# Kernel optimization log

Hardware: AMD Instinct MI355X
Metric: run time of the kernel (lower is better)

## Reference

```python
import jax, jax.numpy as jnp
import numpy as np

HEADS = 8
BLOCK = 32

def setup_inputs() -> dict:
    key = jax.random.key(0)
    ks = jax.random.split(key, 4)
    b, n, d, f = 4, 4096, 1024, 128
    x = jax.random.normal(ks[0], (b, n, d), dtype=jnp.float32)
    w_qkv = jax.random.normal(ks[1], (3 * d, d), dtype=jnp.float32) * (d ** -0.5)
    w_out = jax.random.normal(ks[2], (d, d), dtype=jnp.float32) * (d ** -0.5)
    b_out = jnp.zeros((d,), dtype=jnp.float32)
    proj = jax.random.normal(ks[3], (HEADS, d // HEADS, f), dtype=jnp.float32) * ((d // HEADS) ** -0.5)
    return {"x": x, "w_qkv": w_qkv, "w_out": w_out, "b_out": b_out, "proj": proj}

def reference(x, w_qkv, w_out, b_out, proj):
    b, n, d = x.shape
    h = HEADS
    hd = d // h
    nb = n // BLOCK
    # QKV projection (torch Linear: x @ W.T)
    qkv = x @ w_qkv.T  # (b, n, 3d)
    q, k, v = jnp.split(qkv, 3, axis=-1)
    def to_blocks(t):
        # (b, n, d) -> (b, h, nb, BLOCK, hd)
        return t.reshape(b, n, h, hd).transpose(0, 2, 1, 3).reshape(b, h, nb, BLOCK, hd)
    q, k, v = to_blocks(q), to_blocks(k), to_blocks(v)
    # per-head feature map: elu(x @ proj) + 1
    qp = jax.nn.elu(jnp.einsum('bhcsd,hdf->bhcsf', q, proj)) + 1.0
    kp = jax.nn.elu(jnp.einsum('bhcsd,hdf->bhcsf', k, proj)) + 1.0
    # per-block kv state and normalizer
    kv = jnp.einsum('bhcsf,bhcsd->bhcfd', kp, v)          # (b,h,nb,f,hd)
    num = jnp.einsum('bhcsf,bhcfd->bhcsd', qp, kv)        # (b,h,nb,BLOCK,hd)
    ksum = kp.sum(axis=3)                                 # (b,h,nb,f)
    z = 1.0 / (jnp.einsum('bhcsf,bhcf->bhcs', qp, ksum) + 1e-8)
    out = num * z[..., None]
    # merge blocks and heads: (b,h,nb,BLOCK,hd) -> (b,n,d)
    out = out.reshape(b, h, n, hd).transpose(0, 2, 1, 3).reshape(b, n, d)
    # output projection (dropout inert in eval)
    return out @ w_out.T + b_out
```

## Files before the change

kernel.cpp:

```cpp
#include <hip/hip_runtime.h>
#include <hip/hip_bf16.h>
#include <stdint.h>
#include <stddef.h>

typedef __bf16 bf16_t;
typedef __bf16 bf16x8 __attribute__((ext_vector_type(8)));
typedef __bf16 bf16x4 __attribute__((ext_vector_type(4)));
typedef float  f32x4  __attribute__((ext_vector_type(4)));

static __device__ __forceinline__ f32x4 mfma16x16x32(bf16x8 a, bf16x8 b, f32x4 c) {
  return __builtin_amdgcn_mfma_f32_16x16x32_bf16(a, b, c, 0, 0, 0);
}

static __device__ __forceinline__ void gld_lds16(const void* g, void* l) {
  __builtin_amdgcn_global_load_lds(
      (const __attribute__((address_space(1))) unsigned int*)g,
      (__attribute__((address_space(3))) unsigned int*)l, 16, 0, 0);
}

#define BARW()   __builtin_amdgcn_s_barrier()
#define SCHED0() __builtin_amdgcn_sched_barrier(0)
#define LGKM0()  asm volatile("s_waitcnt lgkmcnt(0)" ::: "memory")
#define LGKMN(n) asm volatile("s_waitcnt lgkmcnt(" #n ")" ::: "memory")
#define VMCNT(n) asm volatile("s_waitcnt vmcnt(" #n ")" ::: "memory")
#define PRIO(p)  __builtin_amdgcn_s_setprio(p)

__global__ __launch_bounds__(256) void cvt_bf16(const float* __restrict__ in,
                                                bf16_t* __restrict__ out, int n) {
  int stride = gridDim.x * blockDim.x;
  for (int i = blockIdx.x * blockDim.x + threadIdx.x; i * 4 < n; i += stride) {
    float4 v = *(const float4*)(in + (size_t)i * 4);
    bf16x4 o;
    o[0] = (bf16_t)v.x; o[1] = (bf16_t)v.y; o[2] = (bf16_t)v.z; o[3] = (bf16_t)v.w;
    *(bf16x4*)(out + (size_t)i * 4) = o;
  }
}

__global__ __launch_bounds__(256) void prep(const float* __restrict__ wqkv,
                                            const float* __restrict__ proj,
                                            const float* __restrict__ wout,
                                            bf16_t* __restrict__ B1t2,
                                            bf16_t* __restrict__ Wv,
                                            bf16_t* __restrict__ W3t) {
  const int b = blockIdx.x;
  const int tid = threadIdx.x;
  if (b >= 256) {
    const float* src = (b < 512) ? wout : (wqkv + (size_t)2048 * 1024);
    bf16_t* dst = (b < 512) ? W3t : Wv;
    size_t off = ((size_t)((b & 255)) * 4096) + tid * 16;
#pragma unroll
    for (int it = 0; it < 4; ++it) {
      float4 v = *(const float4*)(src + off + it * 4);
      bf16x4 o;
      o[0] = (bf16_t)v.x; o[1] = (bf16_t)v.y; o[2] = (bf16_t)v.z; o[3] = (bf16_t)v.w;
      *(bf16x4*)(dst + off + it * 4) = o;
    }
    return;
  }
  const int combo  = b >> 4;
  const int kt     = b & 15;
  const int qk     = combo >> 3;
  const int h      = combo & 7;
  const int klocal = tid & 63;
  const int fg     = tid >> 6;
  const int k      = kt * 64 + klocal;

  const float* wbase = wqkv + ((size_t)(qk * 1024 + h * 128)) * 1024 + k;
  const float* pbase = proj + (size_t)h * 16384 + fg * 32;

  float acc[32];
#pragma unroll
  for (int i = 0; i < 32; ++i) acc[i] = 0.f;

  for (int c = 0; c < 128; ++c) {
    float a = wbase[(size_t)c * 1024];
    const float4* p = (const float4*)(pbase + (size_t)c * 128);
#pragma unroll
    for (int i = 0; i < 8; ++i) {
      float4 pv = p[i];
      acc[i * 4 + 0] += a * pv.x;
      acc[i * 4 + 1] += a * pv.y;
      acc[i * 4 + 2] += a * pv.z;
      acc[i * 4 + 3] += a * pv.w;
    }
  }
  bf16_t* obase = B1t2 + ((size_t)(h * 256 + qk * 128 + fg * 32)) * 1024 + k;
#pragma unroll
  for (int i = 0; i < 32; ++i) obase[(size_t)i * 1024] = (bf16_t)acc[i];
}

#define GEMM_MAINLOOP_DECLS()                                                  \
  const int tid  = threadIdx.x;                                                \
  const int lane = tid & 63;                                                   \
  const int wid  = tid >> 6;                                                   \
  const int wm   = wid >> 2;                                                   \
  const int wn   = wid & 3;                                                    \
  const int lr   = lane & 15;                                                  \
  const int g0   = lane >> 4;                                                  \
  int srow[2], sgl[2];                                                         \
  _Pragma("unroll")                                                            \
  for (int l = 0; l < 2; ++l) {                                                \
    int idx = l * 512 + tid;                                                   \
    srow[l] = idx >> 3;                                                        \
    sgl[l]  = (idx & 7) ^ (srow[l] & 7);                                       \
  }

#define STAGE_T(arr, base, half, kt, K_)                                       \
  {                                                                            \
    const bf16_t* s_ = (base) + (size_t)((half) * 128) * (K_) + (kt) * 64;     \
    bf16_t* d_ = &(arr)[half][0];                                              \
    _Pragma("unroll")                                                          \
    for (int l_ = 0; l_ < 2; ++l_)                                             \
      gld_lds16(s_ + (size_t)srow[l_] * (K_) + sgl[l_] * 8,                    \
                d_ + (l_ * 512 + tid) * 8);                                    \
  }

#define RD_A(buf, qm)                                                          \
  _Pragma("unroll")                                                            \
  for (int t_ = 0; t_ < 4; ++t_) {                                             \
    int r_ = (qm) * 64 + t_ * 16 + lr;                                         \
    _Pragma("unroll")                                                          \
    for (int kh_ = 0; kh_ < 2; ++kh_) {                                        \
      int gl_ = (g0 + kh_ * 4) ^ (r_ & 7);                                     \
      a[t_][kh_] = *(const bf16x8*)(&sA[buf][wm][r_ * 64 + gl_ * 8]);          \
    }                                                                          \
  }
#define RD_B(buf, qn, breg)                                                    \
  _Pragma("unroll")                                                            \
  for (int u_ = 0; u_ < 2; ++u_) {                                             \
    int r_ = (wn & 1) * 64 + (qn) * 32 + u_ * 16 + lr;                         \
    _Pragma("unroll")                                                          \
    for (int kh_ = 0; kh_ < 2; ++kh_) {                                        \
      int gl_ = (g0 + kh_ * 4) ^ (r_ & 7);                                     \
      breg[u_][kh_] = *(const bf16x8*)(&sB[buf][wn >> 1][r_ * 64 + gl_ * 8]);  \
    }                                                                          \
  }
#define MMA(qm, qn, breg)                                                      \
  _Pragma("unroll")                                                            \
  for (int mi_ = 0; mi_ < 4; ++mi_)                                            \
    _Pragma("unroll")                                                          \
    for (int nj_ = 0; nj_ < 2; ++nj_)                                          \
      _Pragma("unroll")                                                        \
      for (int kh_ = 0; kh_ < 2; ++kh_)                                        \
        acc[(qm) * 4 + mi_][(qn) * 2 + nj_] =                                  \
            mfma16x16x32(a[mi_][kh_], breg[nj_][kh_],                          \
                         acc[(qm) * 4 + mi_][(qn) * 2 + nj_]);

#define GEMM_MAINLOOP_BODY(Abase, Bbase, K_, NT_)                              \
  f32x4 acc[8][4] = {};                                                        \
  bf16x8 a[4][2], b0[2][2], b1[2][2];                                          \
  STAGE_T(sA[0], Abase, 0, 0, K_); STAGE_T(sA[0], Abase, 1, 0, K_);            \
  STAGE_T(sB[0], Bbase, 0, 0, K_); STAGE_T(sB[0], Bbase, 1, 0, K_);            \
  STAGE_T(sA[1], Abase, 0, 1, K_); STAGE_T(sA[1], Abase, 1, 1, K_);            \
  STAGE_T(sB[1], Bbase, 0, 1, K_); STAGE_T(sB[1], Bbase, 1, 1, K_);            \
  VMCNT(8);                                                                    \
  BARW();                                                                      \
  _Pragma("unroll 2")                                                          \
  for (int j = 0; j < (NT_); ++j) {                                            \
    const int cur = j & 1;                                                     \
    const bool pf = (j + 2) < (NT_);                                           \
    RD_A(cur, 0);                                                              \
    RD_B(cur, 0, b0);                                                          \
    SCHED0(); LGKMN(8); BARW(); LGKM0(); SCHED0();                             \
    PRIO(1); MMA(0, 0, b0); PRIO(0);                                           \
    SCHED0(); BARW();                                                          \
    RD_B(cur, 1, b1);                                                          \
    SCHED0(); BARW(); LGKM0(); SCHED0();                                       \
    PRIO(1); MMA(0, 1, b1); PRIO(0);                                           \
    SCHED0(); BARW();                                                          \
    RD_A(cur, 1);                                                              \
    if (pf) { STAGE_T(sB[cur], Bbase, 0, j + 2, K_); STAGE_T(sB[cur], Bbase, 1, j + 2, K_); } \
    SCHED0(); LGKMN(4); BARW(); LGKM0(); SCHED0();                             \
    PRIO(1); MMA(1, 1, b1); PRIO(0);                                           \
    SCHED0(); BARW();                                                          \
    if (pf) { STAGE_T(sA[cur], Abase, 0, j + 2, K_); STAGE_T(sA[cur], Abase, 1, j + 2, K_); } \
    SCHED0(); BARW();                                                          \
    PRIO(1); MMA(1, 0, b0); PRIO(0);                                           \
    if (pf) { VMCNT(8); } else { VMCNT(0); }                                   \
    SCHED0(); BARW();                                                          \
  }

template <int EPI>
__global__ __launch_bounds__(512, 2) void gemm256(const bf16_t* __restrict__ A,
                                                  const bf16_t* __restrict__ Bt,
                                                  void* __restrict__ Cout,
                                                  const float* __restrict__ bias,
                                                  int N, int K, int NB) {
  __shared__ __align__(16) bf16_t sA[2][2][8192];
  __shared__ __align__(16) bf16_t sB[2][2][8192];
  GEMM_MAINLOOP_DECLS();

  const int nwg = gridDim.x;
  const int cpx = nwg >> 3;
  const int bid = blockIdx.x;
  const int swz = (bid & 7) * cpx + (bid >> 3);
  const int m0 = (swz / NB) * 256;
  const int n0 = (swz % NB) * 256;
  const int NT = K >> 6;

  const bf16_t* Abase = A  + (size_t)m0 * K;
  const bf16_t* Bbase = Bt + (size_t)n0 * K;

  GEMM_MAINLOOP_BODY(Abase, Bbase, K, NT);

#pragma unroll
  for (int i = 0; i < 8; ++i) {
#pragma unroll
    for (int jn = 0; jn < 4; ++jn) {
      const int n = n0 + wn * 64 + jn * 16 + lr;
#pragma unroll
      for (int r = 0; r < 4; ++r) {
        const int m = m0 + wm * 128 + i * 16 + g0 * 4 + r;
        float v = acc[i][jn][r];
        if constexpr (EPI == 2) {
          ((float*)Cout)[(size_t)m * N + n] = v + bias[n];
        } else {
          ((bf16_t*)Cout)[(size_t)m * N + n] = (bf16_t)v;
        }
      }
    }
  }
}

__global__ __launch_bounds__(512, 2) void gemm_fused(const bf16_t* __restrict__ A,
                                                     const bf16_t* __restrict__ Bt,
                                                     const bf16_t* __restrict__ VtG,
                                                     bf16_t* __restrict__ OUT1) {
  __shared__ __align__(16) bf16_t sA[2][2][8192];
  __shared__ __align__(16) bf16_t sB[2][2][8192];
  GEMM_MAINLOOP_DECLS();

  const int nwg = gridDim.x;
  const int cpx = nwg >> 3;
  const int bid = blockIdx.x;
  const int swz = (bid & 7) * cpx + (bid >> 3);
  const int m0 = (swz >> 3) * 256;
  const int h  = swz & 7;
  const int K  = 1024;
  const int NT = 16;

  const bf16_t* Abase = A  + (size_t)m0 * K;
  const bf16_t* Bbase = Bt + (size_t)(h * 256) * K;

  GEMM_MAINLOOP_BODY(Abase, Bbase, K, NT);

  char* sQb = (char*)(&sA[0][0][0]);
  char* sKb = (char*)(&sB[0][0][0]);

  {
    char* dbase = (wn < 2) ? sQb : sKb;
#pragma unroll
    for (int i = 0; i < 8; ++i)
#pragma unroll
      for (int jn = 0; jn < 4; ++jn)
#pragma unroll
        for (int r = 0; r < 4; ++r) {
          int row = wm * 128 + i * 16 + g0 * 4 + r;
          int col = (wn & 1) * 64 + jn * 16 + lr;
          float v = acc[i][jn][r];
          v = v > 0.f ? v + 1.f : __expf(v);
          int gq = col >> 3;
          int g  = (gq & 8) | ((gq ^ row) & 7);
          *(bf16_t*)(dbase + row * 256 + g * 16 + (col & 7) * 2) = (bf16_t)v;
        }
  }
  LGKM0();
  BARW();

  const int cb = wm * 4 + wn;
  const int rb = cb * 32;
  bf16x8 aS[4][2], bS[4][2];
#pragma unroll
  for (int kh = 0; kh < 4; ++kh) {
#pragma unroll
    for (int t = 0; t < 2; ++t) {
      int row = rb + t * 16 + lr;
      int gq = kh * 4 + g0;
      int g  = (gq & 8) | ((gq ^ row) & 7);
      aS[kh][t] = *(const bf16x8*)(sQb + row * 256 + g * 16);
      bS[kh][t] = *(const bf16x8*)(sKb + row * 256 + g * 16);
    }
  }
  SCHED0(); LGKM0(); BARW();

  {
#pragma unroll
    for (int l = 0; l < 8; ++l) {
      int gd = l * 512 + tid;
      int row = gd >> 5, gcol = gd & 31;
      const bf16_t* src = VtG + (size_t)(h * 128 + row) * 16384 + m0 +
                          ((gcol ^ (row & 7)) * 8);
      gld_lds16(src, sKb + gd * 16);
    }
  }
  SCHED0();

  f32x4 sacc[2][2] = {};
#pragma unroll
  for (int kh = 0; kh < 4; ++kh)
#pragma unroll
    for (int mt = 0; mt < 2; ++mt)
#pragma unroll
      for (int nt = 0; nt < 2; ++nt)
        sacc[mt][nt] = mfma16x16x32(aS[kh][mt], bS[kh][nt], sacc[mt][nt]);

  float zin[2][4];
#pragma unroll
  for (int mt = 0; mt < 2; ++mt)
#pragma unroll
    for (int r = 0; r < 4; ++r) {
      float s = sacc[mt][0][r] + sacc[mt][1][r];
      s += __shfl_xor(s, 1); s += __shfl_xor(s, 2);
      s += __shfl_xor(s, 4); s += __shfl_xor(s, 8);
      zin[mt][r] = 1.0f / (s + 1e-8f);
    }

  char* Pl = sQb;
#pragma unroll
  for (int mt = 0; mt < 2; ++mt)
#pragma unroll
    for (int nt = 0; nt < 2; ++nt)
#pragma unroll
      for (int r = 0; r < 4; ++r) {
        int i = mt * 16 + g0 * 4 + r;
        int jj = nt * 16 + lr;
        *(bf16_t*)(Pl + cb * 2560 + i * 80 + jj * 2) =
            (bf16_t)(sacc[mt][nt][r] * zin[mt][r]);
      }
  LGKM0();
  VMCNT(0);
  BARW();

  bf16x8 aP[2];
#pragma unroll
  for (int mt = 0; mt < 2; ++mt)
    aP[mt] = *(const bf16x8*)(Pl + cb * 2560 + (mt * 16 + lr) * 80 + g0 * 16);
#pragma unroll
  for (int dt = 0; dt < 8; ++dt) {
    int row = dt * 16 + lr;
    int gidx = cb * 4 + g0;
    int g = (gidx & 24) | ((gidx ^ row) & 7);
    bf16x8 bV = *(const bf16x8*)(sKb + row * 512 + g * 16);
#pragma unroll
    for (int mt = 0; mt < 2; ++mt) {
      f32x4 z = {};
      f32x4 o = mfma16x16x32(aP[mt], bV, z);
#pragma unroll
      for (int r = 0; r < 4; ++r) {
        int m = m0 + rb + mt * 16 + g0 * 4 + r;
        int d = h * 128 + dt * 16 + lr;
        OUT1[(size_t)m * 1024 + d] = (bf16_t)o[r];
      }
    }
  }
}

extern "C" void kernel_launch(void* const* d_in, const int* in_sizes, int n_in,
                              void* d_out, int out_size, void* d_ws, size_t ws_size,
                              hipStream_t stream) {
  const float* x     = (const float*)d_in[0];
  const float* w_qkv = (const float*)d_in[1];
  const float* w_out = (const float*)d_in[2];
  const float* b_out = (const float*)d_in[3];
  const float* proj  = (const float*)d_in[4];
  float* out = (float*)d_out;

  char* ws = (char*)d_ws;
  bf16_t* xbf  = (bf16_t*)(ws);
  bf16_t* B1t2 = (bf16_t*)(ws + 33554432);
  bf16_t* Wv   = (bf16_t*)(ws + 37748736);
  bf16_t* W3t  = (bf16_t*)(ws + 39845888);
  bf16_t* VtG  = (bf16_t*)(ws + 41943040);
  bf16_t* OUT1 = (bf16_t*)(ws + 75497472);

  (void)in_sizes; (void)n_in; (void)out_size; (void)ws_size;

  prep<<<768, 256, 0, stream>>>(w_qkv, proj, w_out, B1t2, Wv, W3t);
  cvt_bf16<<<1024, 256, 0, stream>>>(x, xbf, 16777216);
  gemm256<3><<<256, 512, 0, stream>>>(Wv, xbf, (void*)VtG, nullptr, 16384, 1024, 64);
  gemm_fused<<<512, 512, 0, stream>>>(xbf, B1t2, VtG, OUT1);
  gemm256<2><<<256, 512, 0, stream>>>(OUT1, W3t, (void*)out, b_out, 1024, 1024, 4);
}
```

Measured before the change: 235.0 us.

## Fuse x conversion into prep kernel and finer-grained GEMM prefetch staging

Merges the fp32-to-bf16 conversion of x into the weight prep kernel as extra blocks, removing one kernel launch and letting the two conversions run concurrently. It also restructures the GEMM main loop prefetch: the half-tiles of the next stage are issued inside the current iteration, interleaved with the MMA phases, and the waits use a smaller outstanding-load count. The goal is to spread global loads more evenly across compute and shorten the pipeline fill. The changed barrier and wait placement risks stalls or LDS hazards if the waits are not tight enough.

```diff
diff --git a/kernel.cpp b/kernel.cpp
--- a/kernel.cpp
+++ b/kernel.cpp
@@ -21,29 +21,28 @@
 #define BARW()   __builtin_amdgcn_s_barrier()
 #define SCHED0() __builtin_amdgcn_sched_barrier(0)
 #define LGKM0()  asm volatile("s_waitcnt lgkmcnt(0)" ::: "memory")
-#define LGKMN(n) asm volatile("s_waitcnt lgkmcnt(" #n ")" ::: "memory")
 #define VMCNT(n) asm volatile("s_waitcnt vmcnt(" #n ")" ::: "memory")
 #define PRIO(p)  __builtin_amdgcn_s_setprio(p)
-
-__global__ __launch_bounds__(256) void cvt_bf16(const float* __restrict__ in,
-                                                bf16_t* __restrict__ out, int n) {
-  int stride = gridDim.x * blockDim.x;
-  for (int i = blockIdx.x * blockDim.x + threadIdx.x; i * 4 < n; i += stride) {
-    float4 v = *(const float4*)(in + (size_t)i * 4);
-    bf16x4 o;
-    o[0] = (bf16_t)v.x; o[1] = (bf16_t)v.y; o[2] = (bf16_t)v.z; o[3] = (bf16_t)v.w;
-    *(bf16x4*)(out + (size_t)i * 4) = o;
-  }
-}
 
 __global__ __launch_bounds__(256) void prep(const float* __restrict__ wqkv,
                                             const float* __restrict__ proj,
                                             const float* __restrict__ wout,
+                                            const float* __restrict__ x,
                                             bf16_t* __restrict__ B1t2,
                                             bf16_t* __restrict__ Wv,
-                                            bf16_t* __restrict__ W3t) {
+                                            bf16_t* __restrict__ W3t,
+                                            bf16_t* __restrict__ xbf) {
   const int b = blockIdx.x;
   const int tid = threadIdx.x;
+  if (b >= 768) {
+    for (int i = (b - 768) * 256 + tid; i < 4194304; i += 262144) {
+      float4 v = *(const float4*)(x + (size_t)i * 4);
+      bf16x4 o;
+      o[0] = (bf16_t)v.x; o[1] = (bf16_t)v.y; o[2] = (bf16_t)v.z; o[3] = (bf16_t)v.w;
+      *(bf16x4*)(xbf + (size_t)i * 4) = o;
+    }
+    return;
+  }
   if (b >= 256) {
     const float* src = (b < 512) ? wout : (wqkv + (size_t)2048 * 1024);
     bf16_t* dst = (b < 512) ? W3t : Wv;
@@ -149,34 +148,39 @@
 #define GEMM_MAINLOOP_BODY(Abase, Bbase, K_, NT_)                              \
   f32x4 acc[8][4] = {};                                                        \
   bf16x8 a[4][2], b0[2][2], b1[2][2];                                          \
-  STAGE_T(sA[0], Abase, 0, 0, K_); STAGE_T(sA[0], Abase, 1, 0, K_);            \
-  STAGE_T(sB[0], Bbase, 0, 0, K_); STAGE_T(sB[0], Bbase, 1, 0, K_);            \
-  STAGE_T(sA[1], Abase, 0, 1, K_); STAGE_T(sA[1], Abase, 1, 1, K_);            \
-  STAGE_T(sB[1], Bbase, 0, 1, K_); STAGE_T(sB[1], Bbase, 1, 1, K_);            \
-  VMCNT(8);                                                                    \
+  STAGE_T(sB[0], Bbase, 0, 0, K_); STAGE_T(sA[0], Abase, 0, 0, K_);            \
+  STAGE_T(sB[0], Bbase, 1, 0, K_); STAGE_T(sA[0], Abase, 1, 0, K_);            \
+  STAGE_T(sB[1], Bbase, 0, 1, K_); STAGE_T(sA[1], Abase, 0, 1, K_);            \
+  VMCNT(4);                                                                    \
   BARW();                                                                      \
   _Pragma("unroll 2")                                                          \
   for (int j = 0; j < (NT_); ++j) {                                            \
     const int cur = j & 1;                                                     \
-    const bool pf = (j + 2) < (NT_);                                           \
+    const int nxt = cur ^ 1;                                                   \
+                       \
     RD_A(cur, 0);                                                              \
     RD_B(cur, 0, b0);                                                          \
-    SCHED0(); LGKMN(8); BARW(); LGKM0(); SCHED0();                             \
+    if (j + 1 < (NT_)) { STAGE_T(sB[nxt], Bbase, 1, j + 1, K_); }              \
+    SCHED0(); BARW(); LGKM0(); SCHED0();                                       \
     PRIO(1); MMA(0, 0, b0); PRIO(0);                                           \
     SCHED0(); BARW();                                                          \
+                             \
     RD_B(cur, 1, b1);                                                          \
+    if (j + 1 < (NT_)) { STAGE_T(sA[nxt], Abase, 1, j + 1, K_); }              \
     SCHED0(); BARW(); LGKM0(); SCHED0();                                       \
     PRIO(1); MMA(0, 1, b1); PRIO(0);                                           \
     SCHED0(); BARW();                                                          \
+                             \
     RD_A(cur, 1);                                                              \
-    if (pf) { STAGE_T(sB[cur], Bbase, 0, j + 2, K_); STAGE_T(sB[cur], Bbase, 1, j + 2, K_); } \
-    SCHED0(); LGKMN(4); BARW(); LGKM0(); SCHED0();                             \
+    if (j + 2 < (NT_)) { STAGE_T(sB[cur], Bbase, 0, j + 2, K_); }              \
+    SCHED0(); BARW(); LGKM0(); SCHED0();                                       \
     PRIO(1); MMA(1, 1, b1); PRIO(0);                                           \
     SCHED0(); BARW();                                                          \
-    if (pf) { STAGE_T(sA[cur], Abase, 0, j + 2, K_); STAGE_T(sA[cur], Abase, 1, j + 2, K_); } \
+                           \
+    if (j + 2 < (NT_)) { STAGE_T(sA[cur], Abase, 0, j + 2, K_); }              \
     SCHED0(); BARW();                                                          \
     PRIO(1); MMA(1, 0, b0); PRIO(0);                                           \
-    if (pf) { VMCNT(8); } else { VMCNT(0); }                                   \
+    if (j + 2 < (NT_)) { VMCNT(4); } else { VMCNT(0); }                        \
     SCHED0(); BARW();                                                          \
   }
 
@@ -375,8 +379,7 @@
 
   (void)in_sizes; (void)n_in; (void)out_size; (void)ws_size;
 
-  prep<<<768, 256, 0, stream>>>(w_qkv, proj, w_out, B1t2, Wv, W3t);
-  cvt_bf16<<<1024, 256, 0, stream>>>(x, xbf, 16777216);
+  prep<<<1792, 256, 0, stream>>>(w_qkv, proj, w_out, x, B1t2, Wv, W3t, xbf);
   gemm256<3><<<256, 512, 0, stream>>>(Wv, xbf, (void*)VtG, nullptr, 16384, 1024, 64);
   gemm_fused<<<512, 512, 0, stream>>>(xbf, B1t2, VtG, OUT1);
   gemm256<2><<<256, 512, 0, stream>>>(OUT1, W3t, (void*)out, b_out, 1024, 1024, 4);
```

After: 227.7 us. 3.1% less time.

## Fuse V projection into attention GEMM with extra waves and merge bf16 conversion into prep

Applied to the files above, without the earlier changes.

The separate V-projection GEMM and its global VtG buffer are removed. Instead, each head's V weight rows are appended as a third 128-row B slab, so the fused kernel computes Q, K and V features in one main loop. Four extra waves (768 threads per block) own the V tile and write it transposed straight into LDS for the P·V step. The x→bf16 conversion is folded into the prep kernel, cutting total launches from five to three and avoiding a full V write and re-read through HBM. In exchange there is more LDS per block, more register pressure from the larger workgroup, and gemm256 now also reserves the larger sB array.

```diff
diff --git a/kernel.cpp b/kernel.cpp
--- a/kernel.cpp
+++ b/kernel.cpp
@@ -22,38 +22,51 @@
 #define SCHED0() __builtin_amdgcn_sched_barrier(0)
 #define LGKM0()  asm volatile("s_waitcnt lgkmcnt(0)" ::: "memory")
 #define LGKMN(n) asm volatile("s_waitcnt lgkmcnt(" #n ")" ::: "memory")
-#define VMCNT(n) asm volatile("s_waitcnt vmcnt(" #n ")" ::: "memory")
+#define VMCNT_IMM(n) asm volatile("s_waitcnt vmcnt(" #n ")" ::: "memory")
+#define VMCNT(n) VMCNT_IMM(n)
 #define PRIO(p)  __builtin_amdgcn_s_setprio(p)
-
-__global__ __launch_bounds__(256) void cvt_bf16(const float* __restrict__ in,
-                                                bf16_t* __restrict__ out, int n) {
-  int stride = gridDim.x * blockDim.x;
-  for (int i = blockIdx.x * blockDim.x + threadIdx.x; i * 4 < n; i += stride) {
-    float4 v = *(const float4*)(in + (size_t)i * 4);
-    bf16x4 o;
-    o[0] = (bf16_t)v.x; o[1] = (bf16_t)v.y; o[2] = (bf16_t)v.z; o[3] = (bf16_t)v.w;
-    *(bf16x4*)(out + (size_t)i * 4) = o;
-  }
-}
 
 __global__ __launch_bounds__(256) void prep(const float* __restrict__ wqkv,
                                             const float* __restrict__ proj,
                                             const float* __restrict__ wout,
-                                            bf16_t* __restrict__ B1t2,
-                                            bf16_t* __restrict__ Wv,
-                                            bf16_t* __restrict__ W3t) {
+                                            const float* __restrict__ x,
+                                            bf16_t* __restrict__ B1t3,
+                                            bf16_t* __restrict__ W3t,
+                                            bf16_t* __restrict__ xbf) {
   const int b = blockIdx.x;
   const int tid = threadIdx.x;
-  if (b >= 256) {
-    const float* src = (b < 512) ? wout : (wqkv + (size_t)2048 * 1024);
-    bf16_t* dst = (b < 512) ? W3t : Wv;
-    size_t off = ((size_t)((b & 255)) * 4096) + tid * 16;
-#pragma unroll
-    for (int it = 0; it < 4; ++it) {
-      float4 v = *(const float4*)(src + off + it * 4);
+  if (b >= 768) {
+    for (int i = (b - 768) * 256 + tid; i < 4194304; i += 262144) {
+      float4 v = *(const float4*)(x + (size_t)i * 4);
       bf16x4 o;
       o[0] = (bf16_t)v.x; o[1] = (bf16_t)v.y; o[2] = (bf16_t)v.z; o[3] = (bf16_t)v.w;
-      *(bf16x4*)(dst + off + it * 4) = o;
+      *(bf16x4*)(xbf + (size_t)i * 4) = o;
+    }
+    return;
+  }
+  if (b >= 512) {
+    const int d0 = (b - 512) * 4;
+#pragma unroll
+    for (int it = 0; it < 4; ++it) {
+      const int d = d0 + it;
+      const int h = d >> 7, local = d & 127;
+      const float* src = wqkv + (size_t)(2048 + d) * 1024 + tid * 4;
+      bf16_t* dst = B1t3 + (size_t)(h * 384 + 256 + local) * 1024 + tid * 4;
+      float4 v = *(const float4*)src;
+      bf16x4 o;
+      o[0] = (bf16_t)v.x; o[1] = (bf16_t)v.y; o[2] = (bf16_t)v.z; o[3] = (bf16_t)v.w;
+      *(bf16x4*)dst = o;
+    }
+    return;
+  }
+  if (b >= 256) {
+    size_t off = ((size_t)(b & 255) * 4096) + tid * 16;
+#pragma unroll
+    for (int it = 0; it < 4; ++it) {
+      float4 v = *(const float4*)(wout + off + it * 4);
+      bf16x4 o;
+      o[0] = (bf16_t)v.x; o[1] = (bf16_t)v.y; o[2] = (bf16_t)v.z; o[3] = (bf16_t)v.w;
+      *(bf16x4*)(W3t + off + it * 4) = o;
     }
     return;
   }
@@ -84,7 +97,7 @@
       acc[i * 4 + 3] += a * pv.w;
     }
   }
-  bf16_t* obase = B1t2 + ((size_t)(h * 256 + qk * 128 + fg * 32)) * 1024 + k;
+  bf16_t* obase = B1t3 + ((size_t)(h * 384 + qk * 128 + fg * 32)) * 1024 + k;
 #pragma unroll
   for (int i = 0; i < 32; ++i) obase[(size_t)i * 1024] = (bf16_t)acc[i];
 }
@@ -97,16 +110,19 @@
   const int wn   = wid & 3;                                                    \
   const int lr   = lane & 15;                                                  \
   const int g0   = lane >> 4;                                                  \
+  int hA, hB, rB0;                                                             \
+  if (wid < 8) { hA = wid >> 2; hB = (wid & 3) >> 1; rB0 = (wid & 1) * 64; }   \
+  else { int wv_ = wid - 8; hA = wv_ >> 1; hB = 2; rB0 = (wv_ & 1) * 64; }     \
   int srow[2], sgl[2];                                                         \
   _Pragma("unroll")                                                            \
   for (int l = 0; l < 2; ++l) {                                                \
-    int idx = l * 512 + tid;                                                   \
+    int idx = l * 512 + (tid & 511);                                           \
     srow[l] = idx >> 3;                                                        \
     sgl[l]  = (idx & 7) ^ (srow[l] & 7);                                       \
   }
 
 #define STAGE_T(arr, base, half, kt, K_)                                       \
-  {                                                                            \
+  if (tid < 512) {                                                             \
     const bf16_t* s_ = (base) + (size_t)((half) * 128) * (K_) + (kt) * 64;     \
     bf16_t* d_ = &(arr)[half][0];                                              \
     _Pragma("unroll")                                                          \
@@ -122,17 +138,17 @@
     _Pragma("unroll")                                                          \
     for (int kh_ = 0; kh_ < 2; ++kh_) {                                        \
       int gl_ = (g0 + kh_ * 4) ^ (r_ & 7);                                     \
-      a[t_][kh_] = *(const bf16x8*)(&sA[buf][wm][r_ * 64 + gl_ * 8]);          \
+      a[t_][kh_] = *(const bf16x8*)(&sA[buf][hA][r_ * 64 + gl_ * 8]);          \
     }                                                                          \
   }
 #define RD_B(buf, qn, breg)                                                    \
   _Pragma("unroll")                                                            \
   for (int u_ = 0; u_ < 2; ++u_) {                                             \
-    int r_ = (wn & 1) * 64 + (qn) * 32 + u_ * 16 + lr;                         \
+    int r_ = rB0 + (qn) * 32 + u_ * 16 + lr;                                   \
     _Pragma("unroll")                                                          \
     for (int kh_ = 0; kh_ < 2; ++kh_) {                                        \
       int gl_ = (g0 + kh_ * 4) ^ (r_ & 7);                                     \
-      breg[u_][kh_] = *(const bf16x8*)(&sB[buf][wn >> 1][r_ * 64 + gl_ * 8]);  \
+      breg[u_][kh_] = *(const bf16x8*)(&sB[buf][hB][r_ * 64 + gl_ * 8]);       \
     }                                                                          \
   }
 #define MMA(qm, qn, breg)                                                      \
@@ -146,14 +162,16 @@
             mfma16x16x32(a[mi_][kh_], breg[nj_][kh_],                          \
                          acc[(qm) * 4 + mi_][(qn) * 2 + nj_]);
 
-#define GEMM_MAINLOOP_BODY(Abase, Bbase, K_, NT_)                              \
+#define GEMM_MAINLOOP_BODY(Abase, Bbase, K_, NT_, BH, VN)                      \
   f32x4 acc[8][4] = {};                                                        \
   bf16x8 a[4][2], b0[2][2], b1[2][2];                                          \
   STAGE_T(sA[0], Abase, 0, 0, K_); STAGE_T(sA[0], Abase, 1, 0, K_);            \
   STAGE_T(sB[0], Bbase, 0, 0, K_); STAGE_T(sB[0], Bbase, 1, 0, K_);            \
+  if ((BH) > 2) { STAGE_T(sB[0], Bbase, 2, 0, K_); }                           \
   STAGE_T(sA[1], Abase, 0, 1, K_); STAGE_T(sA[1], Abase, 1, 1, K_);            \
   STAGE_T(sB[1], Bbase, 0, 1, K_); STAGE_T(sB[1], Bbase, 1, 1, K_);            \
-  VMCNT(8);                                                                    \
+  if ((BH) > 2) { STAGE_T(sB[1], Bbase, 2, 1, K_); }                           \
+  VMCNT(VN);                                                                   \
   BARW();                                                                      \
   _Pragma("unroll 2")                                                          \
   for (int j = 0; j < (NT_); ++j) {                                            \
@@ -169,25 +187,28 @@
     PRIO(1); MMA(0, 1, b1); PRIO(0);                                           \
     SCHED0(); BARW();                                                          \
     RD_A(cur, 1);                                                              \
-    if (pf) { STAGE_T(sB[cur], Bbase, 0, j + 2, K_); STAGE_T(sB[cur], Bbase, 1, j + 2, K_); } \
+    if (pf) {                                                                  \
+      STAGE_T(sB[cur], Bbase, 0, j + 2, K_);                                   \
+      STAGE_T(sB[cur], Bbase, 1, j + 2, K_);                                   \
+      if ((BH) > 2) { STAGE_T(sB[cur], Bbase, 2, j + 2, K_); }                 \
+    }                                                                          \
     SCHED0(); LGKMN(4); BARW(); LGKM0(); SCHED0();                             \
     PRIO(1); MMA(1, 1, b1); PRIO(0);                                           \
     SCHED0(); BARW();                                                          \
     if (pf) { STAGE_T(sA[cur], Abase, 0, j + 2, K_); STAGE_T(sA[cur], Abase, 1, j + 2, K_); } \
     SCHED0(); BARW();                                                          \
     PRIO(1); MMA(1, 0, b0); PRIO(0);                                           \
-    if (pf) { VMCNT(8); } else { VMCNT(0); }                                   \
+    if (pf) { VMCNT(VN); } else { VMCNT(0); }                                  \
     SCHED0(); BARW();                                                          \
   }
 
-template <int EPI>
 __global__ __launch_bounds__(512, 2) void gemm256(const bf16_t* __restrict__ A,
                                                   const bf16_t* __restrict__ Bt,
                                                   void* __restrict__ Cout,
                                                   const float* __restrict__ bias,
                                                   int N, int K, int NB) {
   __shared__ __align__(16) bf16_t sA[2][2][8192];
-  __shared__ __align__(16) bf16_t sB[2][2][8192];
+  __shared__ __align__(16) bf16_t sB[2][3][8192];
   GEMM_MAINLOOP_DECLS();
 
   const int nwg = gridDim.x;
@@ -201,7 +222,7 @@
   const bf16_t* Abase = A  + (size_t)m0 * K;
   const bf16_t* Bbase = Bt + (size_t)n0 * K;
 
-  GEMM_MAINLOOP_BODY(Abase, Bbase, K, NT);
+  GEMM_MAINLOOP_BODY(Abase, Bbase, K, NT, 2, 8);
 
 #pragma unroll
   for (int i = 0; i < 8; ++i) {
@@ -211,23 +232,17 @@
 #pragma unroll
       for (int r = 0; r < 4; ++r) {
         const int m = m0 + wm * 128 + i * 16 + g0 * 4 + r;
-        float v = acc[i][jn][r];
-        if constexpr (EPI == 2) {
-          ((float*)Cout)[(size_t)m * N + n] = v + bias[n];
-        } else {
-          ((bf16_t*)Cout)[(size_t)m * N + n] = (bf16_t)v;
-        }
+        ((float*)Cout)[(size_t)m * N + n] = acc[i][jn][r] + bias[n];
       }
     }
   }
 }
 
-__global__ __launch_bounds__(512, 2) void gemm_fused(const bf16_t* __restrict__ A,
+__global__ __launch_bounds__(768, 3) void gemm_fused(const bf16_t* __restrict__ A,
                                                      const bf16_t* __restrict__ Bt,
-                                                     const bf16_t* __restrict__ VtG,
                                                      bf16_t* __restrict__ OUT1) {
   __shared__ __align__(16) bf16_t sA[2][2][8192];
-  __shared__ __align__(16) bf16_t sB[2][2][8192];
+  __shared__ __align__(16) bf16_t sB[2][3][8192];
   GEMM_MAINLOOP_DECLS();
 
   const int nwg = gridDim.x;
@@ -240,14 +255,14 @@
   const int NT = 16;
 
   const bf16_t* Abase = A  + (size_t)m0 * K;
-  const bf16_t* Bbase = Bt + (size_t)(h * 256) * K;
-
-  GEMM_MAINLOOP_BODY(Abase, Bbase, K, NT);
+  const bf16_t* Bbase = Bt + (size_t)(h * 384) * K;
+
+  GEMM_MAINLOOP_BODY(Abase, Bbase, K, NT, 3, 10);
 
   char* sQb = (char*)(&sA[0][0][0]);
   char* sKb = (char*)(&sB[0][0][0]);
 
-  {
+  if (wid < 8) {
     char* dbase = (wn < 2) ? sQb : sKb;
 #pragma unroll
     for (int i = 0; i < 8; ++i)
@@ -270,86 +285,95 @@
   const int cb = wm * 4 + wn;
   const int rb = cb * 32;
   bf16x8 aS[4][2], bS[4][2];
-#pragma unroll
-  for (int kh = 0; kh < 4; ++kh) {
-#pragma unroll
-    for (int t = 0; t < 2; ++t) {
-      int row = rb + t * 16 + lr;
-      int gq = kh * 4 + g0;
-      int g  = (gq & 8) | ((gq ^ row) & 7);
-      aS[kh][t] = *(const bf16x8*)(sQb + row * 256 + g * 16);
-      bS[kh][t] = *(const bf16x8*)(sKb + row * 256 + g * 16);
+  if (wid < 8) {
+#pragma unroll
+    for (int kh = 0; kh < 4; ++kh) {
+#pragma unroll
+      for (int t = 0; t < 2; ++t) {
+        int row = rb + t * 16 + lr;
+        int gq = kh * 4 + g0;
+        int g  = (gq & 8) | ((gq ^ row) & 7);
+        aS[kh][t] = *(const bf16x8*)(sQb + row * 256 + g * 16);
+        bS[kh][t] = *(const bf16x8*)(sKb + row * 256 + g * 16);
+      }
     }
   }
   SCHED0(); LGKM0(); BARW();
 
-  {
-#pragma unroll
-    for (int l = 0; l < 8; ++l) {
-      int gd = l * 512 + tid;
-      int row = gd >> 5, gcol = gd & 31;
-      const bf16_t* src = VtG + (size_t)(h * 128 + row) * 16384 + m0 +
-                          ((gcol ^ (row & 7)) * 8);
-      gld_lds16(src, sKb + gd * 16);
-    }
-  }
-  SCHED0();
-
+  float zin[2][4];
   f32x4 sacc[2][2] = {};
-#pragma unroll
-  for (int kh = 0; kh < 4; ++kh)
+  if (wid >= 8) {
+    const int wv = wid - 8;
+    const int mrow0 = (wv >> 1) * 128;
+    const int dcol0 = (wv & 1) * 64;
+#pragma unroll
+    for (int i = 0; i < 8; ++i)
+#pragma unroll
+      for (int jn = 0; jn < 4; ++jn) {
+        int d  = dcol0 + jn * 16 + lr;
+        int mb = mrow0 + i * 16 + g0 * 4;
+        int gm = mb >> 3;
+        int g  = (gm & 24) | ((gm ^ d) & 7);
+        bf16x4 pk;
+#pragma unroll
+        for (int r = 0; r < 4; ++r) pk[r] = (bf16_t)acc[i][jn][r];
+        *(bf16x4*)(sKb + d * 512 + g * 16 + (mb & 7) * 2) = pk;
+      }
+  } else {
+#pragma unroll
+    for (int kh = 0; kh < 4; ++kh)
+#pragma unroll
+      for (int mt = 0; mt < 2; ++mt)
+#pragma unroll
+        for (int nt = 0; nt < 2; ++nt)
+          sacc[mt][nt] = mfma16x16x32(aS[kh][mt], bS[kh][nt], sacc[mt][nt]);
 #pragma unroll
     for (int mt = 0; mt < 2; ++mt)
 #pragma unroll
+      for (int r = 0; r < 4; ++r) {
+        float s = sacc[mt][0][r] + sacc[mt][1][r];
+        s += __shfl_xor(s, 1); s += __shfl_xor(s, 2);
+        s += __shfl_xor(s, 4); s += __shfl_xor(s, 8);
+        zin[mt][r] = 1.0f / (s + 1e-8f);
+      }
+    char* Pl = sQb;
+#pragma unroll
+    for (int mt = 0; mt < 2; ++mt)
+#pragma unroll
       for (int nt = 0; nt < 2; ++nt)
-        sacc[mt][nt] = mfma16x16x32(aS[kh][mt], bS[kh][nt], sacc[mt][nt]);
-
-  float zin[2][4];
-#pragma unroll
-  for (int mt = 0; mt < 2; ++mt)
-#pragma unroll
-    for (int r = 0; r < 4; ++r) {
-      float s = sacc[mt][0][r] + sacc[mt][1][r];
-      s += __shfl_xor(s, 1); s += __shfl_xor(s, 2);
-      s += __shfl_xor(s, 4); s += __shfl_xor(s, 8);
-      zin[mt][r] = 1.0f / (s + 1e-8f);
-    }
-
-  char* Pl = sQb;
-#pragma unroll
-  for (int mt = 0; mt < 2; ++mt)
-#pragma unroll
-    for (int nt = 0; nt < 2; ++nt)
-#pragma unroll
-      for (int r = 0; r < 4; ++r) {
-        int i = mt * 16 + g0 * 4 + r;
-        int jj = nt * 16 + lr;
-        *(bf16_t*)(Pl + cb * 2560 + i * 80 + jj * 2) =
-            (bf16_t)(sacc[mt][nt][r] * zin[mt][r]);
-      }
+#pragma unroll
+        for (int r = 0; r < 4; ++r) {
+          int i = mt * 16 + g0 * 4 + r;
+          int jj = nt * 16 + lr;
+          *(bf16_t*)(Pl + cb * 2560 + i * 80 + jj * 2) =
+              (bf16_t)(sacc[mt][nt][r] * zin[mt][r]);
+        }
+  }
   LGKM0();
-  VMCNT(0);
   BARW();
 
-  bf16x8 aP[2];
-#pragma unroll
-  for (int mt = 0; mt < 2; ++mt)
-    aP[mt] = *(const bf16x8*)(Pl + cb * 2560 + (mt * 16 + lr) * 80 + g0 * 16);
-#pragma unroll
-  for (int dt = 0; dt < 8; ++dt) {
-    int row = dt * 16 + lr;
-    int gidx = cb * 4 + g0;
-    int g = (gidx & 24) | ((gidx ^ row) & 7);
-    bf16x8 bV = *(const bf16x8*)(sKb + row * 512 + g * 16);
-#pragma unroll
-    for (int mt = 0; mt < 2; ++mt) {
-      f32x4 z = {};
-      f32x4 o = mfma16x16x32(aP[mt], bV, z);
-#pragma unroll
-      for (int r = 0; r < 4; ++r) {
-        int m = m0 + rb + mt * 16 + g0 * 4 + r;
-        int d = h * 128 + dt * 16 + lr;
-        OUT1[(size_t)m * 1024 + d] = (bf16_t)o[r];
+  if (wid < 8) {
+    char* Pl = sQb;
+    bf16x8 aP[2];
+#pragma unroll
+    for (int mt = 0; mt < 2; ++mt)
+      aP[mt] = *(const bf16x8*)(Pl + cb * 2560 + (mt * 16 + lr) * 80 + g0 * 16);
+#pragma unroll
+    for (int dt = 0; dt < 8; ++dt) {
+      int row = dt * 16 + lr;
+      int gidx = cb * 4 + g0;
+      int g = (gidx & 24) | ((gidx ^ row) & 7);
+      bf16x8 bV = *(const bf16x8*)(sKb + row * 512 + g * 16);
+#pragma unroll
+      for (int mt = 0; mt < 2; ++mt) {
+        f32x4 z = {};
+        f32x4 o = mfma16x16x32(aP[mt], bV, z);
+#pragma unroll
+        for (int r = 0; r < 4; ++r) {
+          int m = m0 + rb + mt * 16 + g0 * 4 + r;
+          int d = h * 128 + dt * 16 + lr;
+          OUT1[(size_t)m * 1024 + d] = (bf16_t)o[r];
+        }
       }
     }
   }
@@ -367,17 +391,13 @@
 
   char* ws = (char*)d_ws;
   bf16_t* xbf  = (bf16_t*)(ws);
-  bf16_t* B1t2 = (bf16_t*)(ws + 33554432);
-  bf16_t* Wv   = (bf16_t*)(ws + 37748736);
+  bf16_t* B1t3 = (bf16_t*)(ws + 33554432);
   bf16_t* W3t  = (bf16_t*)(ws + 39845888);
-  bf16_t* VtG  = (bf16_t*)(ws + 41943040);
-  bf16_t* OUT1 = (bf16_t*)(ws + 75497472);
+  bf16_t* OUT1 = (bf16_t*)(ws + 41943040);
 
   (void)in_sizes; (void)n_in; (void)out_size; (void)ws_size;
 
-  prep<<<768, 256, 0, stream>>>(w_qkv, proj, w_out, B1t2, Wv, W3t);
-  cvt_bf16<<<1024, 256, 0, stream>>>(x, xbf, 16777216);
-  gemm256<3><<<256, 512, 0, stream>>>(Wv, xbf, (void*)VtG, nullptr, 16384, 1024, 64);
-  gemm_fused<<<512, 512, 0, stream>>>(xbf, B1t2, VtG, OUT1);
-  gemm256<2><<<256, 512, 0, stream>>>(OUT1, W3t, (void*)out, b_out, 1024, 1024, 4);
-}
+  prep<<<1792, 256, 0, stream>>>(w_qkv, proj, w_out, x, B1t3, W3t, xbf);
+  gemm_fused<<<512, 768, 0, stream>>>(xbf, B1t3, OUT1);
+  gemm256<<<256, 512, 0, stream>>>(OUT1, W3t, (void*)out, b_out, 1024, 1024, 4);
+}
```

After: 528.2 us. +124.8%, slower.
